# Kernel optimization log

Hardware: AMD Instinct MI355X
Metric: run time of the kernel (lower is better)

Reference implementation:

```python
import jax, jax.numpy as jnp
import numpy as np

EMBED = 256; HEADS = 8; LEVELS = 4; POINTS = 4; HEAD_DIM = EMBED // HEADS
B = 2; Q = 20000; HP = 128; WP = 128
EPS = 1e-5


def setup_inputs() -> dict:
    key = jax.random.key(0)
    ks = jax.random.split(key, 12)
    s = 1.0 / np.sqrt(EMBED)
    return {
        "query": jax.random.normal(ks[0], (Q, EMBED), jnp.float32),
        "query_spatial_positions": jax.random.uniform(ks[1], (Q, 2), jnp.float32),
        "query_batch_offsets": jnp.array([0, Q // 2, Q], dtype=jnp.int32),
        "stacked_feature_maps": jax.random.normal(ks[2], (B, HP, WP, LEVELS, EMBED), jnp.float32),
        "level_spatial_shapes": jnp.array([[128, 128], [64, 64], [32, 32], [16, 16]], dtype=jnp.int32),
        "norm_gamma": jnp.ones((EMBED,), jnp.float32),
        "norm_beta": jnp.zeros((EMBED,), jnp.float32),
        "W_q": jax.random.normal(ks[3], (EMBED, EMBED), jnp.float32) * s,
        "W_off": jax.random.normal(ks[4], (EMBED, HEADS * LEVELS * POINTS * 2), jnp.float32) * s * 0.1,
        "b_off": jax.random.normal(ks[5], (HEADS * LEVELS * POINTS * 2,), jnp.float32) * 0.5,
        "W_attn": jax.random.normal(ks[6], (EMBED, HEADS * LEVELS * POINTS), jnp.float32) * s,
        "b_attn": jnp.zeros((HEADS * LEVELS * POINTS,), jnp.float32),
        "W_val": jax.random.normal(ks[7], (EMBED, EMBED), jnp.float32) * s,
        "b_val": jnp.zeros((EMBED,), jnp.float32),
        "W_out": jax.random.normal(ks[8], (EMBED, EMBED), jnp.float32) * s,
    }


def _layernorm(x, g, b):
    mu = x.mean(-1, keepdims=True)
    xc = x - mu
    v = (xc * xc).mean(-1, keepdims=True)
    return xc * jax.lax.rsqrt(v + EPS) * g + b


def reference(query, query_spatial_positions, query_batch_offsets, stacked_feature_maps,
              level_spatial_shapes, norm_gamma, norm_beta, W_q, W_off, b_off,
              W_attn, b_attn, W_val, b_val, W_out):
    residual = query
    x = _layernorm(query, norm_gamma, norm_beta)
    x = x @ W_q  # q_in_proj (no bias)

    off = (x @ W_off + b_off).reshape(Q, HEADS, LEVELS, POINTS, 2)
    attn = jax.nn.softmax((x @ W_attn + b_attn).reshape(Q, HEADS, LEVELS * POINTS), axis=-1)
    attn = attn.reshape(Q, HEADS, LEVELS, POINTS)

    # value projection over all levels, split into heads: [B,HP,WP,L,H,HD]
    value = (stacked_feature_maps @ W_val + b_val).reshape(B, HP, WP, LEVELS, HEADS, HEAD_DIM)

    shp = level_spatial_shapes.astype(jnp.float32)  # [L,2] (h,w)
    # normalized ref point + offset scaled by level size -> pixel coords (align_corners=False)
    loc = query_spatial_positions[:, None, None, None, :] + off / shp[None, None, :, None, :]
    pix = loc * shp[None, None, :, None, :] - 0.5  # [Q,H,L,P,2]
    py, px = pix[..., 0], pix[..., 1]
    y0 = jnp.floor(py); x0 = jnp.floor(px)
    wy = py - y0; wx = px - x0
    y0i = y0.astype(jnp.int32); x0i = x0.astype(jnp.int32)

    Hl = level_spatial_shapes[:, 0][None, None, :, None]
    Wl = level_spatial_shapes[:, 1][None, None, :, None]
    b_idx = (jnp.searchsorted(query_batch_offsets, jnp.arange(Q, dtype=jnp.int32), side='right') - 1)[:, None, None, None]
    l_idx = jnp.arange(LEVELS)[None, None, :, None]
    h_idx = jnp.arange(HEADS)[None, :, None, None]

    def gather(yi, xi, w):
        m = (yi >= 0) & (yi < Hl) & (xi >= 0) & (xi < Wl)  # zero-pad outside level extent
        yc = jnp.clip(yi, 0, HP - 1)
        xc = jnp.clip(xi, 0, WP - 1)
        v = value[b_idx, yc, xc, l_idx, h_idx]  # [Q,H,L,P,HD]
        return v * (w * m)[..., None]

    samp = (gather(y0i, x0i, (1 - wy) * (1 - wx))
            + gather(y0i, x0i + 1, (1 - wy) * wx)
            + gather(y0i + 1, x0i, wy * (1 - wx))
            + gather(y0i + 1, x0i + 1, wy * wx))

    out = (attn[..., None] * samp).sum(axis=(2, 3)).reshape(Q, EMBED)
    return out @ W_out + residual
```

## Files before the change

kernel.cpp:

```cpp
#include <hip/hip_runtime.h>
#include <hip/hip_bf16.h>
#include <stdint.h>

#define EMBED 256
#define HEADS 8
#define LEVELS 4
#define POINTS 4
#define HEAD_DIM 32
#define HPAD 128
#define WPAD 128
#define LN_EPS 1e-5f

typedef unsigned short u16;
typedef __attribute__((ext_vector_type(8))) short bf16x8v;
typedef __attribute__((ext_vector_type(4))) float f32x4;

static __device__ __forceinline__ float bu2f(u16 u) {
  return __uint_as_float(((unsigned)u) << 16);
}
static __device__ __forceinline__ u16 f2bu(float f) {
  unsigned x = __float_as_uint(f);
  return (u16)((x + 0x7fffu + ((x >> 16) & 1u)) >> 16);
}
static __device__ __forceinline__ float loadf(const void* p, size_t i, int isbf) {
  return isbf ? bu2f(((const u16*)p)[i]) : ((const float*)p)[i];
}
static __device__ __forceinline__ int imin(int a, int b) { return a < b ? a : b; }

static __device__ __forceinline__ void cp16(const u16* g, u16* l) {
  __builtin_amdgcn_global_load_lds((const __attribute__((address_space(1))) unsigned*)g,
                                   (__attribute__((address_space(3))) unsigned*)l, 16, 0, 0);
}

__global__ __launch_bounds__(256) void detect_kernel(const unsigned* __restrict__ q,
                                                     int* __restrict__ flag) {
  int t = threadIdx.x;
  __shared__ int s[256];
  unsigned u = q[t * 13 + 1];
  unsigned e = (u >> 7) & 0xFF;
  s[t] = (e >= 116 && e <= 130) ? 1 : 0;
  __syncthreads();
  for (int st = 128; st > 0; st >>= 1) { if (t < st) s[t] += s[t + st]; __syncthreads(); }
  if (t == 0) *flag = (s[0] > 200) ? 1 : 0;
}

__global__ __launch_bounds__(384) void boa_kernel(const void* __restrict__ b_off,
                                                  const void* __restrict__ b_attn,
                                                  float* __restrict__ boa,
                                                  const int* __restrict__ dflag) {
  int fl = *dflag;
  int t = threadIdx.x;
  boa[t] = (t < 256) ? loadf(b_off, t, fl) : loadf(b_attn, t - 256, fl);
}

__global__ __launch_bounds__(256) void wtrans_kernel(const void* __restrict__ W,
                                                     u16* __restrict__ Wt,
                                                     int K, int N,
                                                     const int* __restrict__ dflag) {
  int fl = *dflag;
  __shared__ float tile[32][33];
  int tx = threadIdx.x & 31, ty = threadIdx.x >> 5;
  int k0 = blockIdx.x * 32, n0 = blockIdx.y * 32;
#pragma unroll
  for (int j = 0; j < 4; j++) {
    int r = ty + j * 8;
    tile[r][tx] = loadf(W, (size_t)(k0 + r) * N + n0 + tx, fl);
  }
  __syncthreads();
#pragma unroll
  for (int j = 0; j < 4; j++) {
    int n = ty + j * 8;
    Wt[(size_t)(n0 + n) * K + k0 + tx] = f2bu(tile[tx][n]);
  }
}

__global__ __launch_bounds__(256) void ln_kernel(const void* __restrict__ q,
                                                 const void* __restrict__ g,
                                                 const void* __restrict__ be,
                                                 u16* __restrict__ out,
                                                 const int* __restrict__ dflag) {
  int fl = *dflag;
  int row = blockIdx.x;
  int t = threadIdx.x;
  __shared__ float sh[256];
  float v = loadf(q, (size_t)row * EMBED + t, fl);
  sh[t] = v;
  __syncthreads();
  for (int s = 128; s > 0; s >>= 1) { if (t < s) sh[t] += sh[t + s]; __syncthreads(); }
  float mu = sh[0] * (1.f / 256.f);
  __syncthreads();
  float xc = v - mu;
  sh[t] = xc * xc;
  __syncthreads();
  for (int s = 128; s > 0; s >>= 1) { if (t < s) sh[t] += sh[t + s]; __syncthreads(); }
  float r = rsqrtf(sh[0] * (1.f / 256.f) + LN_EPS);
  out[(size_t)row * EMBED + t] = f2bu(xc * r * loadf(g, t, fl) + loadf(be, t, fl));
}

template <int OUTMODE, bool ABF>
__global__ __launch_bounds__(256) void mfma_gemm(const void* __restrict__ A,
                                                 const u16* __restrict__ Bt,
                                                 const void* __restrict__ bias, int BiasC,
                                                 const void* __restrict__ resid,
                                                 void* __restrict__ Cv,
                                                 int M, int N, int K,
                                                 const int* __restrict__ dflag) {
  int fl = *dflag;
  __shared__ u16 As[4096];
  __shared__ u16 Bs[4096];
  int tid = threadIdx.x;
  int m0 = blockIdx.x * 128, n0 = blockIdx.y * 128;
  int wave = tid >> 6, lane = tid & 63;
  int quad = lane >> 4, r16 = lane & 15;
  int wm = (wave >> 1) * 64, wn = (wave & 1) * 64;

  f32x4 acc[4][4];
#pragma unroll
  for (int i = 0; i < 4; i++)
#pragma unroll
    for (int j = 0; j < 4; j++) acc[i][j] = (f32x4){0.f, 0.f, 0.f, 0.f};

  int p0 = tid, p1 = tid + 256;
  int r0 = p0 >> 2, c0 = (p0 & 3) * 8;
  int r1 = p1 >> 2, c1 = (p1 & 3) * 8;
  int ra0 = imin(m0 + r0, M - 1), ra1 = imin(m0 + r1, M - 1);

  const u16*   Ab = (const u16*)A;
  const float* Af = (const float*)A;

  for (int k0 = 0; k0 < K; k0 += 32) {
    __syncthreads();
    if (ABF) {
      cp16(Ab + (size_t)ra0 * K + k0 + c0, &As[p0 * 8]);
      cp16(Ab + (size_t)ra1 * K + k0 + c1, &As[p1 * 8]);
    } else if (fl) {
      *(int4*)&As[p0 * 8] = *(const int4*)(Ab + (size_t)ra0 * K + k0 + c0);
      *(int4*)&As[p1 * 8] = *(const int4*)(Ab + (size_t)ra1 * K + k0 + c1);
    } else {
      float4 f00 = *(const float4*)(Af + (size_t)ra0 * K + k0 + c0);
      float4 f01 = *(const float4*)(Af + (size_t)ra0 * K + k0 + c0 + 4);
      float4 f10 = *(const float4*)(Af + (size_t)ra1 * K + k0 + c1);
      float4 f11 = *(const float4*)(Af + (size_t)ra1 * K + k0 + c1 + 4);
      u16* d0 = &As[p0 * 8];
      d0[0] = f2bu(f00.x); d0[1] = f2bu(f00.y); d0[2] = f2bu(f00.z); d0[3] = f2bu(f00.w);
      d0[4] = f2bu(f01.x); d0[5] = f2bu(f01.y); d0[6] = f2bu(f01.z); d0[7] = f2bu(f01.w);
      u16* d1 = &As[p1 * 8];
      d1[0] = f2bu(f10.x); d1[1] = f2bu(f10.y); d1[2] = f2bu(f10.z); d1[3] = f2bu(f10.w);
      d1[4] = f2bu(f11.x); d1[5] = f2bu(f11.y); d1[6] = f2bu(f11.z); d1[7] = f2bu(f11.w);
    }
    cp16(Bt + (size_t)(n0 + r0) * K + k0 + c0, &Bs[p0 * 8]);
    cp16(Bt + (size_t)(n0 + r1) * K + k0 + c1, &Bs[p1 * 8]);
    __syncthreads();

    bf16x8v a[4], b[4];
#pragma unroll
    for (int i = 0; i < 4; i++)
      a[i] = *(const bf16x8v*)&As[(wm + i * 16 + r16) * 32 + quad * 8];
#pragma unroll
    for (int j = 0; j < 4; j++)
      b[j] = *(const bf16x8v*)&Bs[(wn + j * 16 + r16) * 32 + quad * 8];
#pragma unroll
    for (int i = 0; i < 4; i++)
#pragma unroll
      for (int j = 0; j < 4; j++)
        acc[i][j] = __builtin_amdgcn_mfma_f32_16x16x32_bf16(a[i], b[j], acc[i][j], 0, 0, 0);
  }

  int obf = (OUTMODE == 2) ? fl : OUTMODE;
  int bfl = (BiasC == 2) ? fl : 0;
  if (bias) {
#pragma unroll
    for (int j = 0; j < 4; j++) {
      float bv = loadf(bias, n0 + wn + j * 16 + r16, bfl);
#pragma unroll
      for (int i = 0; i < 4; i++)
#pragma unroll
        for (int reg = 0; reg < 4; reg++) acc[i][j][reg] += bv;
    }
  }

  if (obf) {
    int sl0 = (quad << 4) | ((2 * r16) & 15);
    int sl1 = sl0 + 1;
    bool lohalf = (r16 < 8);
#pragma unroll
    for (int i = 0; i < 4; i++) {
#pragma unroll
      for (int jp = 0; jp < 2; jp++) {
#pragma unroll
        for (int reg = 0; reg < 4; reg++) {
          float vA = acc[i][jp * 2][reg], vB = acc[i][jp * 2 + 1][reg];
          float a0 = __shfl(vA, sl0), a1 = __shfl(vA, sl1);
          float b0 = __shfl(vB, sl0), b1 = __shfl(vB, sl1);
          float lo = lohalf ? a0 : b0;
          float hi = lohalf ? a1 : b1;
          int row = m0 + wm + i * 16 + quad * 4 + reg;
          if (row < M) {
            size_t base = (size_t)row * N + n0 + wn + jp * 32 + 2 * r16;
            if (resid) {
              lo += loadf(resid, base, fl);
              hi += loadf(resid, base + 1, fl);
            }
            unsigned pk = (unsigned)f2bu(lo) | ((unsigned)f2bu(hi) << 16);
            *(unsigned*)((u16*)Cv + base) = pk;
          }
        }
      }
    }
  } else {
#pragma unroll
    for (int j = 0; j < 4; j++) {
      int col = n0 + wn + j * 16 + r16;
#pragma unroll
      for (int i = 0; i < 4; i++) {
#pragma unroll
        for (int reg = 0; reg < 4; reg++) {
          int row = m0 + wm + i * 16 + quad * 4 + reg;
          if (row < M) {
            float v = acc[i][j][reg];
            if (resid) v += loadf(resid, (size_t)row * N + col, fl);
            ((float*)Cv)[(size_t)row * N + col] = v;
          }
        }
      }
    }
  }
}

__global__ __launch_bounds__(256) void sample2_kernel(const float* __restrict__ oa,
                                                      const void* __restrict__ qsp,
                                                      const int* __restrict__ qbo, int nb,
                                                      const int* __restrict__ lss,
                                                      const u16* __restrict__ value,
                                                      u16* __restrict__ samp, int Qn,
                                                      const int* __restrict__ dflag) {
  int fl = *dflag;
  int t = threadIdx.x;
  int q2 = t >> 7;
  int i7 = t & 127;
  int qb = blockIdx.x * 2;
  int q = imin(qb + q2, Qn - 1);

  __shared__ float Loff[2][256];
  __shared__ float Lw[2][128];
  __shared__ int   Lb[2];
  __shared__ int   Co[2][128][4];
  __shared__ float Cw[2][128][4];

  {
    const float* row = oa + (size_t)q * 384;
    float2 v = ((const float2*)row)[i7];
    Loff[q2][i7 * 2]     = v.x;
    Loff[q2][i7 * 2 + 1] = v.y;
    Lw[q2][i7] = row[256 + i7];
  }
  if (t < 2) {
    int qq = imin(qb + t, Qn - 1);
    int b = 0;
    for (int i = 1; i < nb; i++) if (qq >= qbo[i]) b = i;
    Lb[t] = b;
  }
  __syncthreads();

  if (t < 16) {
    int sq = t >> 3, h = t & 7;
    float* w = &Lw[sq][h * 16];
    float mx = w[0];
    for (int i = 1; i < 16; i++) mx = fmaxf(mx, w[i]);
    float s = 0.f;
    for (int i = 0; i < 16; i++) { float e = __expf(w[i] - mx); w[i] = e; s += e; }
    float inv = 1.f / s;
    for (int i = 0; i < 16; i++) w[i] *= inv;
  }
  __syncthreads();

  {
    int h = i7 >> 4, lp = i7 & 15, l = lp >> 2;
    int Hi = lss[l * 2], Wi = lss[l * 2 + 1];
    float Hl = (float)Hi, Wl = (float)Wi;
    float qy = loadf(qsp, (size_t)q * 2, fl);
    float qx = loadf(qsp, (size_t)q * 2 + 1, fl);
    float a  = Lw[q2][i7];
    float oy = Loff[q2][i7 * 2], ox = Loff[q2][i7 * 2 + 1];
    float py = (qy + oy / Hl) * Hl - 0.5f;
    float px = (qx + ox / Wl) * Wl - 0.5f;
    float y0f = floorf(py), x0f = floorf(px);
    float wy = py - y0f, wx = px - x0f;
    int y0 = (int)y0f, x0 = (int)x0f;
    int bbase = Lb[q2] * (HPAD * WPAD * LEVELS * EMBED);
#pragma unroll
    for (int c = 0; c < 4; c++) {
      int yi = y0 + (c >> 1), xi = x0 + (c & 1);
      float w = ((c >> 1) ? wy : 1.f - wy) * ((c & 1) ? wx : 1.f - wx);
      bool ok = (yi >= 0) & (yi < Hi) & (xi >= 0) & (xi < Wi);
      Co[q2][i7][c] = ok ? (bbase + ((yi * WPAD + xi) * LEVELS + l) * EMBED + h * HEAD_DIM) : 0;
      Cw[q2][i7][c] = ok ? (a * w) : 0.f;
    }
  }
  __syncthreads();

  {
    int h = (t >> 4) & 7;
    int d2 = t & 15;
    float ax = 0.f, ay = 0.f;
#pragma unroll
    for (int lp = 0; lp < 16; lp++) {
      int4   o4 = *(const int4*)&Co[q2][h * 16 + lp][0];
      float4 w4 = *(const float4*)&Cw[q2][h * 16 + lp][0];
      unsigned v;
      v = *(const unsigned*)(value + o4.x + d2 * 2);
      ax += w4.x * __uint_as_float(v << 16); ay += w4.x * __uint_as_float(v & 0xffff0000u);
      v = *(const unsigned*)(value + o4.y + d2 * 2);
      ax += w4.y * __uint_as_float(v << 16); ay += w4.y * __uint_as_float(v & 0xffff0000u);
      v = *(const unsigned*)(value + o4.z + d2 * 2);
      ax += w4.z * __uint_as_float(v << 16); ay += w4.z * __uint_as_float(v & 0xffff0000u);
      v = *(const unsigned*)(value + o4.w + d2 * 2);
      ax += w4.w * __uint_as_float(v << 16); ay += w4.w * __uint_as_float(v & 0xffff0000u);
    }
    if (qb + q2 < Qn) {
      unsigned pk = (unsigned)f2bu(ax) | ((unsigned)f2bu(ay) << 16);
      *(unsigned*)(samp + (size_t)(qb + q2) * 256 + h * 32 + d2 * 2) = pk;
    }
  }
}

extern "C" void kernel_launch(void* const* d_in, const int* in_sizes, int n_in,
                              void* d_out, int out_size, void* d_ws, size_t ws_size,
                              hipStream_t stream) {
  const void* query  = d_in[0];
  const void* qsp    = d_in[1];
  const int*  qbo    = (const int*)d_in[2];
  const void* sfm    = d_in[3];
  const int*  lss    = (const int*)d_in[4];
  const void* gamma  = d_in[5];
  const void* beta   = d_in[6];
  const void* W_q    = d_in[7];
  const void* W_off  = d_in[8];
  const void* b_off  = d_in[9];
  const void* W_attn = d_in[10];
  const void* b_attn = d_in[11];
  const void* W_val  = d_in[12];
  const void* b_val  = d_in[13];
  const void* W_out  = d_in[14];

  const int Q  = in_sizes[0] / EMBED;
  const int nb = in_sizes[2] - 1;
  const int MV = in_sizes[3] / EMBED;

  char* ws = (char*)d_ws;
  size_t o = 0;
  auto alloc = [&](size_t bytes) { size_t r = o; o = (o + bytes + 255) & ~(size_t)255; return r; };
  u16*   xln   = (u16*)(ws + alloc((size_t)Q * EMBED * sizeof(u16)));
  u16*   x     = (u16*)(ws + alloc((size_t)Q * EMBED * sizeof(u16)));
  float* oaw   = (float*)(ws + alloc((size_t)Q * 384 * sizeof(float)));
  u16*   valw  = (u16*)(ws + alloc((size_t)MV * EMBED * sizeof(u16)));
  u16*   sampw = (u16*)(ws + alloc((size_t)Q * EMBED * sizeof(u16)));
  u16*   wtq   = (u16*)(ws + alloc(256 * 256 * sizeof(u16)));
  u16*   wtoa  = (u16*)(ws + alloc(384 * 256 * sizeof(u16)));
  u16*   wtval = (u16*)(ws + alloc(256 * 256 * sizeof(u16)));
  u16*   wtout = (u16*)(ws + alloc(256 * 256 * sizeof(u16)));
  float* boa   = (float*)(ws + alloc(384 * sizeof(float)));
  int*   dflag = (int*)(ws + alloc(256));
  (void)ws_size;

  detect_kernel<<<1, 256, 0, stream>>>((const unsigned*)query, dflag);
  boa_kernel<<<1, 384, 0, stream>>>(b_off, b_attn, boa, dflag);

  wtrans_kernel<<<dim3(8, 8), 256, 0, stream>>>(W_q,    wtq,              256, 256, dflag);
  wtrans_kernel<<<dim3(8, 8), 256, 0, stream>>>(W_off,  wtoa,             256, 256, dflag);
  wtrans_kernel<<<dim3(8, 4), 256, 0, stream>>>(W_attn, wtoa + 256 * 256, 256, 128, dflag);
  wtrans_kernel<<<dim3(8, 8), 256, 0, stream>>>(W_val,  wtval,            256, 256, dflag);
  wtrans_kernel<<<dim3(8, 8), 256, 0, stream>>>(W_out,  wtout,            256, 256, dflag);

  ln_kernel<<<Q, 256, 0, stream>>>(query, gamma, beta, xln, dflag);

  const int GQ = (Q + 127) / 128;
  mfma_gemm<1, true><<<dim3(GQ, 2), 256, 0, stream>>>(xln, wtq, nullptr, 0, nullptr, x, Q, 256, 256, dflag);
  mfma_gemm<0, true><<<dim3(GQ, 3), 256, 0, stream>>>(x, wtoa, boa, 0, nullptr, oaw, Q, 384, 256, dflag);
  mfma_gemm<1, false><<<dim3(MV / 128, 2), 256, 0, stream>>>(sfm, wtval, b_val, 2, nullptr, valw, MV, 256, 256, dflag);
  sample2_kernel<<<(Q + 1) / 2, 256, 0, stream>>>(oaw, qsp, qbo, nb, lss, valw, sampw, Q, dflag);
  mfma_gemm<2, true><<<dim3(GQ, 2), 256, 0, stream>>>(sampw, wtout, nullptr, 0, query, d_out, Q, 256, 256, dflag);
}
```

Baseline: 431.4 us.

## Triple-buffer GEMM LDS tiles with prefetch and XOR-swizzled layout

Converts the MFMA GEMM main loop to a triple-buffered software pipeline: the next K-tile's global-to-LDS copies are issued right after the barrier, so they overlap the MFMAs on the current tile, and only one barrier per iteration remains. It also XOR-swizzles the 16-byte column chunks in LDS by row to reduce bank conflicts on the fragment reads. In exchange the kernel uses three times the LDS, which may lower occupancy, and it relies on a full vmcnt/lgkmcnt wait plus sched_barrier hints.

```diff
diff --git a/kernel.cpp b/kernel.cpp
--- a/kernel.cpp
+++ b/kernel.cpp
@@ -106,8 +106,8 @@
                                                  int M, int N, int K,
                                                  const int* __restrict__ dflag) {
   int fl = *dflag;
-  __shared__ u16 As[4096];
-  __shared__ u16 Bs[4096];
+  __shared__ u16 As[3][4096];
+  __shared__ u16 Bs[3][4096];
   int tid = threadIdx.x;
   int m0 = blockIdx.x * 128, n0 = blockIdx.y * 128;
   int wave = tid >> 6, lane = tid & 63;
@@ -121,49 +121,70 @@
     for (int j = 0; j < 4; j++) acc[i][j] = (f32x4){0.f, 0.f, 0.f, 0.f};
 
   int p0 = tid, p1 = tid + 256;
-  int r0 = p0 >> 2, c0 = (p0 & 3) * 8;
-  int r1 = p1 >> 2, c1 = (p1 & 3) * 8;
+  int r0 = p0 >> 2, c0 = ((p0 & 3) ^ (r0 & 3)) * 8;
+  int r1 = p1 >> 2, c1 = ((p1 & 3) ^ (r1 & 3)) * 8;
   int ra0 = imin(m0 + r0, M - 1), ra1 = imin(m0 + r1, M - 1);
 
   const u16*   Ab = (const u16*)A;
   const float* Af = (const float*)A;
-
-  for (int k0 = 0; k0 < K; k0 += 32) {
-    __syncthreads();
-    if (ABF) {
-      cp16(Ab + (size_t)ra0 * K + k0 + c0, &As[p0 * 8]);
-      cp16(Ab + (size_t)ra1 * K + k0 + c1, &As[p1 * 8]);
-    } else if (fl) {
-      *(int4*)&As[p0 * 8] = *(const int4*)(Ab + (size_t)ra0 * K + k0 + c0);
-      *(int4*)&As[p1 * 8] = *(const int4*)(Ab + (size_t)ra1 * K + k0 + c1);
+  const bool adma = ABF || (fl != 0);
+
+  float4 fA0, fA1, fA2, fA3;
+
+  auto issueTile = [&](int k0, int buf) {
+    if (adma) {
+      cp16(Ab + (size_t)ra0 * K + k0 + c0, &As[buf][p0 * 8]);
+      cp16(Ab + (size_t)ra1 * K + k0 + c1, &As[buf][p1 * 8]);
     } else {
-      float4 f00 = *(const float4*)(Af + (size_t)ra0 * K + k0 + c0);
-      float4 f01 = *(const float4*)(Af + (size_t)ra0 * K + k0 + c0 + 4);
-      float4 f10 = *(const float4*)(Af + (size_t)ra1 * K + k0 + c1);
-      float4 f11 = *(const float4*)(Af + (size_t)ra1 * K + k0 + c1 + 4);
-      u16* d0 = &As[p0 * 8];
-      d0[0] = f2bu(f00.x); d0[1] = f2bu(f00.y); d0[2] = f2bu(f00.z); d0[3] = f2bu(f00.w);
-      d0[4] = f2bu(f01.x); d0[5] = f2bu(f01.y); d0[6] = f2bu(f01.z); d0[7] = f2bu(f01.w);
-      u16* d1 = &As[p1 * 8];
-      d1[0] = f2bu(f10.x); d1[1] = f2bu(f10.y); d1[2] = f2bu(f10.z); d1[3] = f2bu(f10.w);
-      d1[4] = f2bu(f11.x); d1[5] = f2bu(f11.y); d1[6] = f2bu(f11.z); d1[7] = f2bu(f11.w);
-    }
-    cp16(Bt + (size_t)(n0 + r0) * K + k0 + c0, &Bs[p0 * 8]);
-    cp16(Bt + (size_t)(n0 + r1) * K + k0 + c1, &Bs[p1 * 8]);
-    __syncthreads();
+      fA0 = *(const float4*)(Af + (size_t)ra0 * K + k0 + c0);
+      fA1 = *(const float4*)(Af + (size_t)ra0 * K + k0 + c0 + 4);
+      fA2 = *(const float4*)(Af + (size_t)ra1 * K + k0 + c1);
+      fA3 = *(const float4*)(Af + (size_t)ra1 * K + k0 + c1 + 4);
+    }
+    cp16(Bt + (size_t)(n0 + r0) * K + k0 + c0, &Bs[buf][p0 * 8]);
+    cp16(Bt + (size_t)(n0 + r1) * K + k0 + c1, &Bs[buf][p1 * 8]);
+  };
+  auto writeA = [&](int buf) {
+    if (!adma) {
+      u16* d0 = &As[buf][p0 * 8];
+      d0[0] = f2bu(fA0.x); d0[1] = f2bu(fA0.y); d0[2] = f2bu(fA0.z); d0[3] = f2bu(fA0.w);
+      d0[4] = f2bu(fA1.x); d0[5] = f2bu(fA1.y); d0[6] = f2bu(fA1.z); d0[7] = f2bu(fA1.w);
+      u16* d1 = &As[buf][p1 * 8];
+      d1[0] = f2bu(fA2.x); d1[1] = f2bu(fA2.y); d1[2] = f2bu(fA2.z); d1[3] = f2bu(fA2.w);
+      d1[4] = f2bu(fA3.x); d1[5] = f2bu(fA3.y); d1[6] = f2bu(fA3.z); d1[7] = f2bu(fA3.w);
+    }
+  };
+
+  issueTile(0, 0);
+  const int nt = K >> 5;
+  int cur = 0;
+  const int rq = r16 & 3;
+  const int foff = (quad ^ rq) * 8;
+
+  for (int t = 0; t < nt; ++t) {
+    writeA(cur);
+    asm volatile("s_waitcnt vmcnt(0) lgkmcnt(0)" ::: "memory");
+    __builtin_amdgcn_sched_barrier(0);
+    __builtin_amdgcn_s_barrier();
+    __builtin_amdgcn_sched_barrier(0);
+
+    int nx = cur + 1; if (nx == 3) nx = 0;
+    if (t + 1 < nt) issueTile((t + 1) << 5, nx);
 
     bf16x8v a[4], b[4];
 #pragma unroll
     for (int i = 0; i < 4; i++)
-      a[i] = *(const bf16x8v*)&As[(wm + i * 16 + r16) * 32 + quad * 8];
+      a[i] = *(const bf16x8v*)&As[cur][(wm + i * 16 + r16) * 32 + foff];
 #pragma unroll
     for (int j = 0; j < 4; j++)
-      b[j] = *(const bf16x8v*)&Bs[(wn + j * 16 + r16) * 32 + quad * 8];
+      b[j] = *(const bf16x8v*)&Bs[cur][(wn + j * 16 + r16) * 32 + foff];
 #pragma unroll
     for (int i = 0; i < 4; i++)
 #pragma unroll
       for (int j = 0; j < 4; j++)
         acc[i][j] = __builtin_amdgcn_mfma_f32_16x16x32_bf16(a[i], b[j], acc[i][j], 0, 0, 0);
+    __builtin_amdgcn_sched_barrier(0);
+    cur = nx;
   }
 
   int obf = (OUTMODE == 2) ? fl : OUTMODE;
```

Result: no change. 436.4 us (+1.2%).

## Add dedicated value-projection GEMM with full-K LDS A tile and packed bf16 stores

Applied to the files above, without the earlier changes.

Replaces the generic mfma_gemm used for the value projection with a specialized 512-thread kernel. Each block loads a full 128x256 A tile into LDS with an XOR swizzle, converting fp32 to bf16 on load, so the A matrix is read once instead of once per N-half. B fragments are read directly from global memory. Results are shuffled so each lane writes packed bf16 pairs, giving wider, coalesced stores. The 64KB of LDS per block and the higher register use may limit occupancy.

```diff
diff --git a/kernel.cpp b/kernel.cpp
--- a/kernel.cpp
+++ b/kernel.cpp
@@ -227,6 +227,123 @@
   }
 }
 
+__global__ __launch_bounds__(512) void val_gemm(const void* __restrict__ A,
+                                                const u16* __restrict__ Bt,
+                                                const void* __restrict__ bias,
+                                                u16* __restrict__ Cv,
+                                                int M, const int* __restrict__ dflag) {
+  int fl = *dflag;
+  __shared__ u16 As[128 * 256];
+  int tid = threadIdx.x;
+  int m0 = blockIdx.x * 128;
+  int wave = tid >> 6, lane = tid & 63;
+  int quad = lane >> 4, r16 = lane & 15;
+  int wm = (wave >> 2) * 64, wn = (wave & 3) * 64;
+
+  if (fl) {
+    const uint4* A16 = (const uint4*)A;
+#pragma unroll
+    for (int i = 0; i < 8; i++) {
+      int g = i * 512 + tid;
+      int r = g >> 5, c = g & 31;
+      int rg = imin(m0 + r, M - 1);
+      uint4 v = A16[(size_t)rg * 32 + c];
+      *(uint4*)&As[r * 256 + ((c ^ (r & 7)) * 8)] = v;
+    }
+  } else {
+    const float4* A4 = (const float4*)A;
+#pragma unroll
+    for (int p = 0; p < 2; p++) {
+      float4 f[8];
+#pragma unroll
+      for (int q = 0; q < 8; q++) {
+        int g = (p * 8 + q) * 512 + tid;
+        int rg = imin(m0 + (g >> 6), M - 1);
+        f[q] = A4[(size_t)rg * 64 + (g & 63)];
+      }
+#pragma unroll
+      for (int q = 0; q < 8; q++) {
+        int g = (p * 8 + q) * 512 + tid;
+        int r = g >> 6, cw = g & 63;
+        int c = cw >> 1, sub = cw & 1;
+        uint2 w;
+        w.x = (unsigned)f2bu(f[q].x) | ((unsigned)f2bu(f[q].y) << 16);
+        w.y = (unsigned)f2bu(f[q].z) | ((unsigned)f2bu(f[q].w) << 16);
+        *(uint2*)&As[r * 256 + ((c ^ (r & 7)) * 8) + sub * 4] = w;
+      }
+    }
+  }
+  __syncthreads();
+
+  f32x4 acc[4][4];
+#pragma unroll
+  for (int i = 0; i < 4; i++)
+#pragma unroll
+    for (int j = 0; j < 4; j++) acc[i][j] = (f32x4){0.f, 0.f, 0.f, 0.f};
+
+  int arow[4], arl[4];
+#pragma unroll
+  for (int i = 0; i < 4; i++) {
+    arow[i] = (wm + i * 16 + r16) * 256;
+    arl[i]  = (wm + i * 16 + r16) & 7;
+  }
+  const u16* bbase[4];
+#pragma unroll
+  for (int j = 0; j < 4; j++)
+    bbase[j] = Bt + (size_t)(wn + j * 16 + r16) * 256 + quad * 8;
+
+#pragma unroll
+  for (int t = 0; t < 8; t++) {
+    bf16x8v b[4];
+#pragma unroll
+    for (int j = 0; j < 4; j++)
+      b[j] = *(const bf16x8v*)(bbase[j] + t * 32);
+    bf16x8v a[4];
+#pragma unroll
+    for (int i = 0; i < 4; i++) {
+      int chunk = ((t << 2) | quad) ^ arl[i];
+      a[i] = *(const bf16x8v*)&As[arow[i] + chunk * 8];
+    }
+#pragma unroll
+    for (int i = 0; i < 4; i++)
+#pragma unroll
+      for (int j = 0; j < 4; j++)
+        acc[i][j] = __builtin_amdgcn_mfma_f32_16x16x32_bf16(a[i], b[j], acc[i][j], 0, 0, 0);
+  }
+
+#pragma unroll
+  for (int j = 0; j < 4; j++) {
+    float bv = loadf(bias, wn + j * 16 + r16, fl);
+#pragma unroll
+    for (int i = 0; i < 4; i++)
+#pragma unroll
+      for (int reg = 0; reg < 4; reg++) acc[i][j][reg] += bv;
+  }
+  int sl0 = (quad << 4) | ((2 * r16) & 15);
+  int sl1 = sl0 + 1;
+  bool lohalf = (r16 < 8);
+#pragma unroll
+  for (int i = 0; i < 4; i++) {
+#pragma unroll
+    for (int jp = 0; jp < 2; jp++) {
+#pragma unroll
+      for (int reg = 0; reg < 4; reg++) {
+        float vA = acc[i][jp * 2][reg], vB = acc[i][jp * 2 + 1][reg];
+        float a0 = __shfl(vA, sl0), a1 = __shfl(vA, sl1);
+        float b0 = __shfl(vB, sl0), b1 = __shfl(vB, sl1);
+        float lo = lohalf ? a0 : b0;
+        float hi = lohalf ? a1 : b1;
+        int row = m0 + wm + i * 16 + quad * 4 + reg;
+        if (row < M) {
+          size_t base = (size_t)row * 256 + wn + jp * 32 + 2 * r16;
+          unsigned pk = (unsigned)f2bu(lo) | ((unsigned)f2bu(hi) << 16);
+          *(unsigned*)(Cv + base) = pk;
+        }
+      }
+    }
+  }
+}
+
 __global__ __launch_bounds__(256) void sample2_kernel(const float* __restrict__ oa,
                                                       const void* __restrict__ qsp,
                                                       const int* __restrict__ qbo, int nb,
@@ -377,7 +494,7 @@
   const int GQ = (Q + 127) / 128;
   mfma_gemm<1, true><<<dim3(GQ, 2), 256, 0, stream>>>(xln, wtq, nullptr, 0, nullptr, x, Q, 256, 256, dflag);
   mfma_gemm<0, true><<<dim3(GQ, 3), 256, 0, stream>>>(x, wtoa, boa, 0, nullptr, oaw, Q, 384, 256, dflag);
-  mfma_gemm<1, false><<<dim3(MV / 128, 2), 256, 0, stream>>>(sfm, wtval, b_val, 2, nullptr, valw, MV, 256, 256, dflag);
+  val_gemm<<<dim3(MV / 128), 512, 0, stream>>>(sfm, wtval, b_val, valw, MV, dflag);
   sample2_kernel<<<(Q + 1) / 2, 256, 0, stream>>>(oaw, qsp, qbo, nb, lss, valw, sampw, Q, dflag);
   mfma_gemm<2, true><<<dim3(GQ, 2), 256, 0, stream>>>(sampw, wtout, nullptr, 0, query, d_out, Q, 256, 256, dflag);
 }
```

After: 428.1 us. Within noise of the previous version (-0.8%).
